# Performance work log

Hardware: AMD Instinct MI355X
Metric: run time of the kernel (lower is better)

Reference implementation:

```python
import jax, jax.numpy as jnp
import numpy as np

SIGMA = 45.0
N, M, D = 4096, 4096, 1024


def setup_inputs() -> dict:
    key = jax.random.key(0)
    k1, k2 = jax.random.split(key)
    inputs = jax.random.normal(k1, (N, D), dtype=jnp.float32)
    samples = jax.random.normal(k2, (M, D), dtype=jnp.float32)
    return {"inputs": inputs, "samples": samples}


def _sq_dists(x, y):
    # ||x_i||^2 + ||y_j||^2 - 2 x_i.y_j  -> [N, M]
    prod = x @ y.T
    xs = jnp.sum(x * x, axis=1)[:, None]
    ys = jnp.sum(y * y, axis=1)[None, :]
    return xs + ys - 2.0 * prod


def reference(inputs, samples):
    n = inputs.shape[0]
    m = samples.shape[0]
    x = inputs.reshape(n, -1)
    y = samples.reshape(m, -1)
    inv_s2 = 1.0 / (SIGMA ** 2)

    k_xx = _sq_dists(x, x)
    k_yy = _sq_dists(y, y)
    k_xy = _sq_dists(x, y)

    # unbiased MMD: exclude diagonal terms of k_xx, k_yy
    exx = jnp.exp(-k_xx * inv_s2)
    eyy = jnp.exp(-k_yy * inv_s2)
    exy = jnp.exp(-k_xy * inv_s2)

    mmd = (jnp.sum(exx) - jnp.sum(jnp.exp(-jnp.diag(k_xx) * inv_s2))) / (n * (n - 1))
    mmd = mmd + (jnp.sum(eyy) - jnp.sum(jnp.exp(-jnp.diag(k_yy) * inv_s2))) / (m * (m - 1))
    mmd = mmd - 2.0 / (n * m) * jnp.sum(exy)
    return mmd
```

## Files before the change

### kernel.cpp

```cpp
#include <hip/hip_runtime.h>
#include <math.h>


typedef _Float16 f16_t;
typedef _Float16 f16x4 __attribute__((ext_vector_type(4)));
typedef _Float16 f16x8 __attribute__((ext_vector_type(8)));
typedef float floatx4 __attribute__((ext_vector_type(4)));

#define NROWS 4096
#define MROWS 4096
#define DDIM  1024
#define BM    256
#define BN    128
#define BK    32
#define NKT   (DDIM / BK)
#define NTR   (NROWS / BM)
#define NTC   (NROWS / BN)
#define XXB   272
#define NBLK  (2 * XXB + NTR * NTC)

__global__ __launch_bounds__(256) void convert_kernel(
    const float* __restrict__ X, const float* __restrict__ Y,
    f16_t* __restrict__ Xh, f16_t* __restrict__ Yh,
    float* __restrict__ nx, float* __restrict__ ny) {
    const int wid  = threadIdx.x >> 6;
    const int lane = threadIdx.x & 63;
    const int row  = blockIdx.x * 4 + wid;
    const float* src;
    f16_t* dst;
    float* nrm;
    int r;
    if (row < NROWS) {
        r = row;         src = X + (size_t)r * DDIM;
        dst = Xh + (size_t)r * DDIM;  nrm = nx;
    } else {
        r = row - NROWS; src = Y + (size_t)r * DDIM;
        dst = Yh + (size_t)r * DDIM;  nrm = ny;
    }
    const float4* s4 = (const float4*)src;
    f16x4* d4 = (f16x4*)dst;
    float s = 0.f;
    #pragma unroll
    for (int c = 0; c < 4; c++) {
        float4 v = s4[c * 64 + lane];
        f16x4 h;
        h[0] = (f16_t)v.x; h[1] = (f16_t)v.y;
        h[2] = (f16_t)v.z; h[3] = (f16_t)v.w;
        d4[c * 64 + lane] = h;
        float h0 = (float)h[0], h1 = (float)h[1];
        float h2 = (float)h[2], h3 = (float)h[3];
        s += h0 * h0 + h1 * h1 + h2 * h2 + h3 * h3;
    }
    #pragma unroll
    for (int off = 32; off > 0; off >>= 1) s += __shfl_down(s, off);
    if (lane == 0) nrm[r] = s;
}

#define STAGE(tt_) do {                                                        \
    const int slot_ = (tt_) & 3;                                               \
    const int kk_ = (((tt_) < NKT) ? (tt_) : (NKT - 1)) * BK;                  \
    __builtin_amdgcn_global_load_lds(                                          \
        (const __attribute__((address_space(1))) void*)(gA + kk_),             \
        (__attribute__((address_space(3))) void*)(&ldsA[slot_][wave * 1024]),  \
        16, 0, 0);                                                             \
    __builtin_amdgcn_global_load_lds(                                          \
        (const __attribute__((address_space(1))) void*)(gA + kk_ + 16 * DDIM), \
        (__attribute__((address_space(3))) void*)(&ldsA[slot_][wave * 1024 + 512]), \
        16, 0, 0);                                                             \
    __builtin_amdgcn_global_load_lds(                                          \
        (const __attribute__((address_space(1))) void*)(gB + kk_),             \
        (__attribute__((address_space(3))) void*)(&ldsB[slot_][wave * 512]),   \
        16, 0, 0);                                                             \
  } while (0)

__global__ __launch_bounds__(512, 2) void mmd_mfma(
    const f16_t* __restrict__ Xh, const f16_t* __restrict__ Yh,
    const float* __restrict__ nx, const float* __restrict__ ny,
    double* __restrict__ partials) {
    __shared__ __align__(16) f16_t ldsA[4][BM * BK];
    __shared__ __align__(16) f16_t ldsB[4][BN * BK];
    __shared__ double wred[8];

    const int b = blockIdx.x;
    const f16_t *Aptr, *Bptr;
    const float *nAp, *nBp;
    double coef;
    if (b < 2 * XXB) {
        int u = (b < XXB) ? b : b - XXB;
        int i = 0;
        while (u >= NTC - 2 * i) { u -= NTC - 2 * i; i++; }
        const int ti = i, tj = 2 * i + u;
        const double w = (tj >= 2 * i + 2) ? 2.0 : 1.0;
        const f16_t* base;
        const float* nb_;
        double denom;
        if (b < XXB) { base = Xh; nb_ = nx; denom = (double)NROWS * (double)(NROWS - 1); }
        else         { base = Yh; nb_ = ny; denom = (double)MROWS * (double)(MROWS - 1); }
        Aptr = base + (size_t)ti * BM * DDIM;
        Bptr = base + (size_t)tj * BN * DDIM;
        nAp = nb_ + ti * BM;  nBp = nb_ + tj * BN;
        coef = w / denom;
    } else {
        const int u = b - 2 * XXB;
        const int ti = u >> 5, tj = u & 31;
        Aptr = Xh + (size_t)ti * BM * DDIM;
        Bptr = Yh + (size_t)tj * BN * DDIM;
        nAp = nx + ti * BM;  nBp = ny + tj * BN;
        coef = -2.0 / ((double)NROWS * (double)MROWS);
    }

    const int tid  = threadIdx.x;
    const int wave = tid >> 6;
    const int lane = tid & 63;
    const int wm   = wave >> 1;
    const int wn   = wave & 1;
    const int m    = lane & 15;
    const int quad = lane >> 4;
    const int sw8  = (quad ^ ((m >> 1) & 3)) * 8;
    const int aoff = (wm * 64 + m) * BK + sw8;
    const int boff = (wn * 64 + m) * BK + sw8;

    const int lr = lane >> 2;
    const int lc = (lane & 3) ^ ((lane >> 3) & 3);
    const f16_t* gA = Aptr + (size_t)(wave * 32 + lr) * DDIM + lc * 8;
    const f16_t* gB = Bptr + (size_t)(wave * 16 + lr) * DDIM + lc * 8;

    floatx4 acc[4][4];
    #pragma unroll
    for (int i = 0; i < 4; i++)
        #pragma unroll
        for (int j = 0; j < 4; j++) acc[i][j] = (floatx4){0.f, 0.f, 0.f, 0.f};

    STAGE(0); STAGE(1); STAGE(2);
    asm volatile("s_waitcnt vmcnt(6)" ::: "memory");
    __builtin_amdgcn_s_barrier();

    for (int t = 0; t < NKT; ++t) {
        const int slot = t & 3;
        f16x8 ah[4], bh[4];
        #pragma unroll
        for (int s = 0; s < 4; s++) {
            ah[s] = *(const f16x8*)&ldsA[slot][aoff + s * 16 * BK];
            bh[s] = *(const f16x8*)&ldsB[slot][boff + s * 16 * BK];
        }
        STAGE(t + 3);
        asm volatile("s_waitcnt vmcnt(6)" ::: "memory");
        __builtin_amdgcn_s_barrier();
        __builtin_amdgcn_s_setprio(1);
        #pragma unroll
        for (int i = 0; i < 4; i++)
            #pragma unroll
            for (int j = 0; j < 4; j++)
                acc[i][j] = __builtin_amdgcn_mfma_f32_16x16x32_f16(ah[i], bh[j], acc[i][j], 0, 0, 0);
        __builtin_amdgcn_s_setprio(0);
        __builtin_amdgcn_s_barrier();
    }

    const float inv_s2 = 1.0f / 2025.0f;
    float nbv[4];
    #pragma unroll
    for (int j = 0; j < 4; j++) nbv[j] = nBp[wn * 64 + j * 16 + m];
    float lsum = 0.f;
    #pragma unroll
    for (int i = 0; i < 4; i++) {
        floatx4 na4 = *(const floatx4*)&nAp[wm * 64 + i * 16 + quad * 4];
        #pragma unroll
        for (int j = 0; j < 4; j++)
            #pragma unroll
            for (int r = 0; r < 4; r++) {
                float arg = (2.f * acc[i][j][r] - na4[r] - nbv[j]) * inv_s2;
                lsum += __expf(arg);
            }
    }

    double d = (double)lsum;
    #pragma unroll
    for (int off = 32; off > 0; off >>= 1) d += __shfl_down(d, off);
    if (lane == 0) wred[wave] = d;
    __syncthreads();
    if (tid == 0) {
        double s = 0.0;
        #pragma unroll
        for (int w = 0; w < 8; w++) s += wred[w];
        partials[b] = s * coef;
    }
}

__global__ __launch_bounds__(256) void final_reduce(const double* __restrict__ partials,
                                                    float* __restrict__ out) {
    __shared__ double red[256];
    int t = threadIdx.x;
    double s = 0.0;
    for (int i = t; i < NBLK; i += 256) s += partials[i];
    red[t] = s;
    __syncthreads();
    for (int off = 128; off > 0; off >>= 1) {
        if (t < off) red[t] += red[t + off];
        __syncthreads();
    }
    if (t == 0) {
        double mmd = red[0] - 1.0 / (double)(NROWS - 1) - 1.0 / (double)(MROWS - 1);
        out[0] = (float)mmd;
    }
}

extern "C" void kernel_launch(void* const* d_in, const int* in_sizes, int n_in,
                              void* d_out, int out_size, void* d_ws, size_t ws_size,
                              hipStream_t stream) {
    const float* X = (const float*)d_in[0];
    const float* Y = (const float*)d_in[1];
    float* out = (float*)d_out;

    char* p = (char*)d_ws;
    double* partials = (double*)p;            p += ((size_t)NBLK * sizeof(double) + 255) & ~255ULL;
    float* nx = (float*)p;                    p += (size_t)NROWS * sizeof(float);
    float* ny = (float*)p;                    p += (size_t)MROWS * sizeof(float);
    f16_t* Xh = (f16_t*)p;                    p += (size_t)NROWS * DDIM * sizeof(f16_t);
    f16_t* Yh = (f16_t*)p;

    convert_kernel<<<(NROWS + MROWS) / 4, 256, 0, stream>>>(X, Y, Xh, Yh, nx, ny);
    mmd_mfma<<<NBLK, 512, 0, stream>>>(Xh, Yh, nx, ny, partials);
    final_reduce<<<1, 256, 0, stream>>>(partials, out);
}
```

Baseline: 181.2 us.

## Store fp16 operands in K-panel-major layout for contiguous tile loads

The convert kernel now writes the fp16 copies of X and Y as K-panels of width BK, laid out [panel][row][BK], in place of row-major. The GEMM's global-to-LDS loads then fetch each k-step's tile from one contiguous region rather than rows strided by DDIM. The goal is better DRAM/TLB locality and fewer scattered cache lines per stage. In exchange, the convert kernel's stores become strided across panels.

```diff
diff --git a/kernel.cpp b/kernel.cpp
--- a/kernel.cpp
+++ b/kernel.cpp
@@ -14,6 +14,7 @@
 #define BN    128
 #define BK    32
 #define NKT   (DDIM / BK)
+#define PSTRIDE (4096 * BK)
 #define NTR   (NROWS / BM)
 #define NTC   (NROWS / BN)
 #define XXB   272
@@ -21,24 +22,23 @@
 
 __global__ __launch_bounds__(256) void convert_kernel(
     const float* __restrict__ X, const float* __restrict__ Y,
-    f16_t* __restrict__ Xh, f16_t* __restrict__ Yh,
+    f16_t* __restrict__ Xp, f16_t* __restrict__ Yp,
     float* __restrict__ nx, float* __restrict__ ny) {
     const int wid  = threadIdx.x >> 6;
     const int lane = threadIdx.x & 63;
     const int row  = blockIdx.x * 4 + wid;
     const float* src;
-    f16_t* dst;
+    f16_t* dstp;
     float* nrm;
     int r;
     if (row < NROWS) {
         r = row;         src = X + (size_t)r * DDIM;
-        dst = Xh + (size_t)r * DDIM;  nrm = nx;
+        dstp = Xp;  nrm = nx;
     } else {
         r = row - NROWS; src = Y + (size_t)r * DDIM;
-        dst = Yh + (size_t)r * DDIM;  nrm = ny;
+        dstp = Yp;  nrm = ny;
     }
     const float4* s4 = (const float4*)src;
-    f16x4* d4 = (f16x4*)dst;
     float s = 0.f;
     #pragma unroll
     for (int c = 0; c < 4; c++) {
@@ -46,7 +46,8 @@
         f16x4 h;
         h[0] = (f16_t)v.x; h[1] = (f16_t)v.y;
         h[2] = (f16_t)v.z; h[3] = (f16_t)v.w;
-        d4[c * 64 + lane] = h;
+        *(f16x4*)(dstp + (size_t)(c * 8 + (lane >> 3)) * PSTRIDE
+                       + (size_t)r * BK + (lane & 7) * 4) = h;
         float h0 = (float)h[0], h1 = (float)h[1];
         float h2 = (float)h[2], h3 = (float)h[3];
         s += h0 * h0 + h1 * h1 + h2 * h2 + h3 * h3;
@@ -58,13 +59,13 @@
 
 #define STAGE(tt_) do {                                                        \
     const int slot_ = (tt_) & 3;                                               \
-    const int kk_ = (((tt_) < NKT) ? (tt_) : (NKT - 1)) * BK;                  \
+    const size_t kk_ = (size_t)(((tt_) < NKT) ? (tt_) : (NKT - 1)) * PSTRIDE;  \
     __builtin_amdgcn_global_load_lds(                                          \
         (const __attribute__((address_space(1))) void*)(gA + kk_),             \
         (__attribute__((address_space(3))) void*)(&ldsA[slot_][wave * 1024]),  \
         16, 0, 0);                                                             \
     __builtin_amdgcn_global_load_lds(                                          \
-        (const __attribute__((address_space(1))) void*)(gA + kk_ + 16 * DDIM), \
+        (const __attribute__((address_space(1))) void*)(gA + kk_ + 16 * BK),   \
         (__attribute__((address_space(3))) void*)(&ldsA[slot_][wave * 1024 + 512]), \
         16, 0, 0);                                                             \
     __builtin_amdgcn_global_load_lds(                                          \
@@ -74,7 +75,7 @@
   } while (0)
 
 __global__ __launch_bounds__(512, 2) void mmd_mfma(
-    const f16_t* __restrict__ Xh, const f16_t* __restrict__ Yh,
+    const f16_t* __restrict__ Xp, const f16_t* __restrict__ Yp,
     const float* __restrict__ nx, const float* __restrict__ ny,
     double* __restrict__ partials) {
     __shared__ __align__(16) f16_t ldsA[4][BM * BK];
@@ -82,8 +83,9 @@
     __shared__ double wred[8];
 
     const int b = blockIdx.x;
-    const f16_t *Aptr, *Bptr;
+    const f16_t *Abase, *Bbase;
     const float *nAp, *nBp;
+    int arow0, brow0;
     double coef;
     if (b < 2 * XXB) {
         int u = (b < XXB) ? b : b - XXB;
@@ -94,17 +96,17 @@
         const f16_t* base;
         const float* nb_;
         double denom;
-        if (b < XXB) { base = Xh; nb_ = nx; denom = (double)NROWS * (double)(NROWS - 1); }
-        else         { base = Yh; nb_ = ny; denom = (double)MROWS * (double)(MROWS - 1); }
-        Aptr = base + (size_t)ti * BM * DDIM;
-        Bptr = base + (size_t)tj * BN * DDIM;
+        if (b < XXB) { base = Xp; nb_ = nx; denom = (double)NROWS * (double)(NROWS - 1); }
+        else         { base = Yp; nb_ = ny; denom = (double)MROWS * (double)(MROWS - 1); }
+        Abase = base; Bbase = base;
+        arow0 = ti * BM;  brow0 = tj * BN;
         nAp = nb_ + ti * BM;  nBp = nb_ + tj * BN;
         coef = w / denom;
     } else {
         const int u = b - 2 * XXB;
         const int ti = u >> 5, tj = u & 31;
-        Aptr = Xh + (size_t)ti * BM * DDIM;
-        Bptr = Yh + (size_t)tj * BN * DDIM;
+        Abase = Xp; Bbase = Yp;
+        arow0 = ti * BM;  brow0 = tj * BN;
         nAp = nx + ti * BM;  nBp = ny + tj * BN;
         coef = -2.0 / ((double)NROWS * (double)MROWS);
     }
@@ -122,8 +124,8 @@
 
     const int lr = lane >> 2;
     const int lc = (lane & 3) ^ ((lane >> 3) & 3);
-    const f16_t* gA = Aptr + (size_t)(wave * 32 + lr) * DDIM + lc * 8;
-    const f16_t* gB = Bptr + (size_t)(wave * 16 + lr) * DDIM + lc * 8;
+    const f16_t* gA = Abase + (size_t)(arow0 + wave * 32 + lr) * BK + lc * 8;
+    const f16_t* gB = Bbase + (size_t)(brow0 + wave * 16 + lr) * BK + lc * 8;
 
     floatx4 acc[4][4];
     #pragma unroll
@@ -215,10 +217,10 @@
     double* partials = (double*)p;            p += ((size_t)NBLK * sizeof(double) + 255) & ~255ULL;
     float* nx = (float*)p;                    p += (size_t)NROWS * sizeof(float);
     float* ny = (float*)p;                    p += (size_t)MROWS * sizeof(float);
-    f16_t* Xh = (f16_t*)p;                    p += (size_t)NROWS * DDIM * sizeof(f16_t);
-    f16_t* Yh = (f16_t*)p;
-
-    convert_kernel<<<(NROWS + MROWS) / 4, 256, 0, stream>>>(X, Y, Xh, Yh, nx, ny);
-    mmd_mfma<<<NBLK, 512, 0, stream>>>(Xh, Yh, nx, ny, partials);
+    f16_t* Xp = (f16_t*)p;                    p += (size_t)NROWS * DDIM * sizeof(f16_t);
+    f16_t* Yp = (f16_t*)p;
+
+    convert_kernel<<<(NROWS + MROWS) / 4, 256, 0, stream>>>(X, Y, Xp, Yp, nx, ny);
+    mmd_mfma<<<NBLK, 512, 0, stream>>>(Xp, Yp, nx, ny, partials);
     final_reduce<<<1, 256, 0, stream>>>(partials, out);
 }
```

After: 165.5 us. 8.7% less time.
